# Kernel tuning notes

Measured on AMD Instinct MI355X. Metric: run time of the kernel, lower is better.

The kernel has to match this reference:

```python
import jax, jax.numpy as jnp
import numpy as np

B, S, D, H = 4, 2048, 768, 12
DH = D // H          # 64 head dim
DF = 4 * D           # 3072 FFN hidden
EPS = 1e-5


def setup_inputs() -> dict:
    key = jax.random.key(0)
    ks = jax.random.split(key, 16)
    s = 0.02
    inp = {
        "Q": jax.random.normal(ks[0], (B, S, D), jnp.float32),
        "K": jax.random.normal(ks[1], (B, S, D), jnp.float32),
        "V": jax.random.normal(ks[2], (B, S, D), jnp.float32),
        "Wq": s * jax.random.normal(ks[3], (D, D), jnp.float32),
        "bq": jnp.zeros((D,), jnp.float32),
        "Wk": s * jax.random.normal(ks[4], (D, D), jnp.float32),
        "bk": jnp.zeros((D,), jnp.float32),
        "Wv": s * jax.random.normal(ks[5], (D, D), jnp.float32),
        "bv": jnp.zeros((D,), jnp.float32),
        "Wo": s * jax.random.normal(ks[6], (D, D), jnp.float32),
        "bo": jnp.zeros((D,), jnp.float32),
        "ln_g": jnp.ones((D,), jnp.float32),
        "ln_b": jnp.zeros((D,), jnp.float32),
        "W1": s * jax.random.normal(ks[7], (D, DF), jnp.float32),
        "b1": jnp.zeros((DF,), jnp.float32),
        "W2": s * jax.random.normal(ks[8], (DF, D), jnp.float32),
        "b2": jnp.zeros((D,), jnp.float32),
    }
    return inp


def _split_heads(x):  # [B,S,D] -> [B,H,S,DH]
    return x.reshape(B, S, H, DH).transpose(0, 2, 1, 3)


def _layernorm(x, g, b):
    mu = jnp.mean(x, axis=-1, keepdims=True)
    var = jnp.mean(jnp.square(x - mu), axis=-1, keepdims=True)
    return (x - mu) * jax.lax.rsqrt(var + EPS) * g + b


def reference(Q, K, V, Wq, bq, Wk, bk, Wv, bv, Wo, bo, ln_g, ln_b, W1, b1, W2, b2):
    q = _split_heads(Q @ Wq + bq)            # [B,H,S,DH]
    k = _split_heads(K @ Wk + bk)
    v = _split_heads(V @ Wv + bv)
    scale = 1.0 / jnp.sqrt(jnp.asarray(DH, q.dtype))
    scores = jnp.einsum("bhqd,bhkd->bhqk", q, k) * scale   # [B,H,S,S]
    attn = jax.nn.softmax(scores, axis=-1)
    ctx = jnp.einsum("bhqk,bhkd->bhqd", attn, v)            # [B,H,S,DH]
    ctx = ctx.transpose(0, 2, 1, 3).reshape(B, S, D)
    attn_out = ctx @ Wo + bo
    h = _layernorm(Q + attn_out, ln_g, ln_b)                # residual + LN
    ff = jax.nn.gelu(h @ W1 + b1, approximate=False) @ W2 + b2
    return ff
```

## Files before the change

kernel.cpp:

```cpp
#include <hip/hip_runtime.h>
#include <hip/hip_bf16.h>
#include <math.h>

#define Bsz 4
#define Ssz 2048
#define Dsz 768
#define Hn  12
#define DHn 64
#define DFn 3072
#define NTOK (Bsz*Ssz)
#define EPSL 1e-5f

typedef __attribute__((ext_vector_type(8))) short bf16x8;
typedef __attribute__((ext_vector_type(4))) float f32x4;

__device__ __forceinline__ unsigned short f2bf(float f) {
    unsigned int u = __float_as_uint(f);
    u += 0x7fffu + ((u >> 16) & 1u);
    return (unsigned short)(u >> 16);
}
__device__ __forceinline__ float bf2f(unsigned short h) {
    return __uint_as_float(((unsigned int)h) << 16);
}

__device__ __forceinline__ void swizzle_mn(int bid, int mtot, int nb, int& m, int& n)
{
    const int xcd = bid & 7;
    const int idx = bid >> 3;
    m = xcd * (mtot >> 3) + idx / nb;
    n = idx % nb;
}

__global__ __launch_bounds__(256)
void wsplit_k(const float* __restrict__ W, unsigned short* __restrict__ Wh,
              unsigned short* __restrict__ Wl, int K, int N)
{
    __shared__ float tile[32][33];
    const int n0 = blockIdx.x * 32, k0 = blockIdx.y * 32;
    const int x = threadIdx.x, y = threadIdx.y;
    #pragma unroll
    for (int i = 0; i < 4; i++)
        tile[y + 8 * i][x] = W[(size_t)(k0 + y + 8 * i) * N + n0 + x];
    __syncthreads();
    #pragma unroll
    for (int i = 0; i < 4; i++) {
        float v = tile[x][y + 8 * i];
        unsigned short hb = f2bf(v);
        size_t o = (size_t)(n0 + y + 8 * i) * K + k0 + x;
        Wh[o] = hb;
        Wl[o] = f2bf(v - bf2f(hb));
    }
}

__global__ __launch_bounds__(256)
void presplit_k(const float* __restrict__ Qf, const float* __restrict__ Kf,
                const float* __restrict__ Vf,
                unsigned short* __restrict__ Qh, unsigned short* __restrict__ Ql,
                unsigned short* __restrict__ Kh, unsigned short* __restrict__ Kl,
                unsigned short* __restrict__ Vh)
{
    const int blocksPerSeg = (NTOK * Dsz) / 2048;
    const int seg = blockIdx.x / blocksPerSeg;
    const int idx = ((blockIdx.x % blocksPerSeg) * 256 + threadIdx.x) * 8;
    const float* src = (seg == 0) ? Qf : (seg == 1) ? Kf : Vf;

    float4 a = *(const float4*)(src + idx);
    float4 b = *(const float4*)(src + idx + 4);
    float fv[8] = {a.x, a.y, a.z, a.w, b.x, b.y, b.z, b.w};

    bf16x8 h8, l8;
    #pragma unroll
    for (int e = 0; e < 8; e++) {
        unsigned short hb = f2bf(fv[e]);
        h8[e] = (short)hb;
        l8[e] = (short)f2bf(fv[e] - bf2f(hb));
    }
    unsigned short* Hp = (seg == 0) ? Qh : (seg == 1) ? Kh : Vh;
    *(bf16x8*)(Hp + idx) = h8;
    if (seg < 2) {
        unsigned short* Lp = (seg == 0) ? Ql : Kl;
        *(bf16x8*)(Lp + idx) = l8;
    }
}

__global__ __launch_bounds__(256)
void qkv_mfma(const unsigned short* __restrict__ Qsh, const unsigned short* __restrict__ Qsl,
              const unsigned short* __restrict__ Ksh, const unsigned short* __restrict__ Ksl,
              const unsigned short* __restrict__ Vsh,
              const unsigned short* __restrict__ Wqh, const unsigned short* __restrict__ Wql,
              const unsigned short* __restrict__ Wkh, const unsigned short* __restrict__ Wkl,
              const unsigned short* __restrict__ Wvh, const unsigned short* __restrict__ Wvl,
              const float* __restrict__ bq, const float* __restrict__ bk,
              const float* __restrict__ bv,
              unsigned short* __restrict__ qh, unsigned short* __restrict__ ql,
              unsigned short* __restrict__ kh, unsigned short* __restrict__ kl,
              unsigned short* __restrict__ vout)
{
    __shared__ short smem[16384];
    short* As_h = smem;
    short* As_l = smem + 4096;
    short* Bs_h = smem + 8192;
    short* Bs_l = smem + 12288;

    const int t    = threadIdx.x;
    const int lane = t & 63;
    const int w    = t >> 6;
    const int wm   = w >> 1;
    const int wn   = w & 1;

    int m_tile, nblk;
    swizzle_mn(blockIdx.x, 192, 6, m_tile, nblk);
    const int which = m_tile / 64;
    const int m0    = (m_tile % 64) * 128;
    const int n0    = nblk * 128;

    const unsigned short* Ah = (which == 0) ? Qsh : (which == 1) ? Ksh : Vsh;
    const unsigned short* Al = (which == 0) ? Qsl : Ksl;
    const unsigned short* Bh = (which == 0) ? Wqh : (which == 1) ? Wkh : Wvh;
    const unsigned short* Bl = (which == 0) ? Wql : (which == 1) ? Wkl : Wvl;
    const float* bias = (which == 0) ? bq : (which == 1) ? bk : bv;

    f32x4 acc[4][4];
    #pragma unroll
    for (int i = 0; i < 4; i++)
        #pragma unroll
        for (int j = 0; j < 4; j++)
            acc[i][j] = (f32x4){0.f, 0.f, 0.f, 0.f};

    const int fr = lane & 15;
    const int q8 = (lane >> 4) * 8;

    for (int k0 = 0; k0 < Dsz; k0 += 32) {
        __syncthreads();
        #pragma unroll
        for (int it = 0; it < 2; it++) {
            const int p   = t + 256 * it;
            const int row = p >> 2;
            const int c8  = (p & 3) * 8;
            const unsigned short* ga_h = Ah + (size_t)(m0 + row) * Dsz + k0 + c8;
            const unsigned short* gb_h = Bh + (size_t)(n0 + row) * Dsz + k0 + c8;
            __builtin_amdgcn_global_load_lds((const __attribute__((address_space(1))) void*)ga_h,
                (__attribute__((address_space(3))) void*)(As_h + p * 8), 16, 0, 0);
            __builtin_amdgcn_global_load_lds((const __attribute__((address_space(1))) void*)gb_h,
                (__attribute__((address_space(3))) void*)(Bs_h + p * 8), 16, 0, 0);
            if (which < 2) {
                const unsigned short* ga_l = Al + (size_t)(m0 + row) * Dsz + k0 + c8;
                const unsigned short* gb_l = Bl + (size_t)(n0 + row) * Dsz + k0 + c8;
                __builtin_amdgcn_global_load_lds((const __attribute__((address_space(1))) void*)ga_l,
                    (__attribute__((address_space(3))) void*)(As_l + p * 8), 16, 0, 0);
                __builtin_amdgcn_global_load_lds((const __attribute__((address_space(1))) void*)gb_l,
                    (__attribute__((address_space(3))) void*)(Bs_l + p * 8), 16, 0, 0);
            }
        }
        __syncthreads();

        bf16x8 a_h[4], a_l[4], b_h[4], b_l[4];
        #pragma unroll
        for (int i = 0; i < 4; i++) {
            const int ra = (wm * 64 + i * 16 + fr) * 32 + q8;
            const int rb = (wn * 64 + i * 16 + fr) * 32 + q8;
            a_h[i] = *(const bf16x8*)&As_h[ra];
            b_h[i] = *(const bf16x8*)&Bs_h[rb];
            if (which < 2) {
                a_l[i] = *(const bf16x8*)&As_l[ra];
                b_l[i] = *(const bf16x8*)&Bs_l[rb];
            }
        }
        if (which < 2) {
            #pragma unroll
            for (int i = 0; i < 4; i++)
                #pragma unroll
                for (int j = 0; j < 4; j++) {
                    acc[i][j] = __builtin_amdgcn_mfma_f32_16x16x32_bf16(a_l[i], b_h[j], acc[i][j], 0, 0, 0);
                    acc[i][j] = __builtin_amdgcn_mfma_f32_16x16x32_bf16(a_h[i], b_l[j], acc[i][j], 0, 0, 0);
                    acc[i][j] = __builtin_amdgcn_mfma_f32_16x16x32_bf16(a_h[i], b_h[j], acc[i][j], 0, 0, 0);
                }
        } else {
            #pragma unroll
            for (int i = 0; i < 4; i++)
                #pragma unroll
                for (int j = 0; j < 4; j++)
                    acc[i][j] = __builtin_amdgcn_mfma_f32_16x16x32_bf16(a_h[i], b_h[j], acc[i][j], 0, 0, 0);
        }
    }

    const int quad = lane >> 4;
    #pragma unroll
    for (int i = 0; i < 4; i++)
        #pragma unroll
        for (int j = 0; j < 4; j++) {
            const int n  = n0 + wn * 64 + j * 16 + fr;
            const float bn = bias[n];
            const int hh = n >> 6, dh = n & 63;
            #pragma unroll
            for (int r = 0; r < 4; r++) {
                const int m = m0 + wm * 64 + i * 16 + quad * 4 + r;
                const int bb = m >> 11, s = m & 2047;
                const size_t o = (((size_t)bb * Hn + hh) * Ssz + s) * DHn + dh;
                float v = acc[i][j][r] + bn;
                if (which == 0) {
                    v *= 0.125f;
                    unsigned short hb = f2bf(v);
                    qh[o] = hb; ql[o] = f2bf(v - bf2f(hb));
                } else if (which == 1) {
                    unsigned short hb = f2bf(v);
                    kh[o] = hb; kl[o] = f2bf(v - bf2f(hb));
                } else {
                    vout[o] = f2bf(v);
                }
            }
        }
}

__global__ __launch_bounds__(256)
void vtrans_k(const unsigned short* __restrict__ src, unsigned short* __restrict__ dst)
{
    __shared__ unsigned short tl[32][33];
    const int s0 = blockIdx.x * 32;
    const int d0 = blockIdx.y * 32;
    const int hd = blockIdx.z;
    const int x = threadIdx.x, y = threadIdx.y;
    const size_t base = (size_t)hd * Ssz * DHn;
    #pragma unroll
    for (int i = 0; i < 4; i++)
        tl[y + 8 * i][x] = src[base + (size_t)(s0 + y + 8 * i) * DHn + d0 + x];
    __syncthreads();
    #pragma unroll
    for (int i = 0; i < 4; i++)
        dst[base + (size_t)(d0 + y + 8 * i) * Ssz + s0 + x] = tl[x][y + 8 * i];
}

template<int MODE, bool ASPLIT, bool BSPLIT, int BM>
__global__ __launch_bounds__(256)
void gemm_mfma(const unsigned short* __restrict__ Ah, const unsigned short* __restrict__ Al,
               const unsigned short* __restrict__ Bh, const unsigned short* __restrict__ Bl,
               const float* __restrict__ bias, const float* __restrict__ res,
               float* __restrict__ Cf, unsigned short* __restrict__ Cb,
               int M, int N, int K)
{
    constexpr int MI = BM / 32;
    __shared__ short smem[16384];
    short* As_h = smem;
    short* As_l = smem + 4096;
    short* Bs_h = smem + 8192;
    short* Bs_l = smem + 12288;

    const int t    = threadIdx.x;
    const int lane = t & 63;
    const int w    = t >> 6;
    const int wm   = w >> 1;
    const int wn   = w & 1;

    int mt, nt_;
    swizzle_mn(blockIdx.x, M / BM, N >> 7, mt, nt_);
    const int m0 = mt * BM;
    const int n0 = nt_ * 128;

    f32x4 acc[MI][4];
    #pragma unroll
    for (int i = 0; i < MI; i++)
        #pragma unroll
        for (int j = 0; j < 4; j++)
            acc[i][j] = (f32x4){0.f, 0.f, 0.f, 0.f};

    const int fr = lane & 15;
    const int q8 = (lane >> 4) * 8;

    for (int k0 = 0; k0 < K; k0 += 32) {
        __syncthreads();
        #pragma unroll
        for (int it = 0; it < BM / 64; it++) {
            const int p   = t + 256 * it;
            const int row = p >> 2;
            const int c8  = (p & 3) * 8;
            const unsigned short* ga_h = Ah + (size_t)(m0 + row) * K + k0 + c8;
            __builtin_amdgcn_global_load_lds((const __attribute__((address_space(1))) void*)ga_h,
                (__attribute__((address_space(3))) void*)(As_h + p * 8), 16, 0, 0);
            if (ASPLIT) {
                const unsigned short* ga_l = Al + (size_t)(m0 + row) * K + k0 + c8;
                __builtin_amdgcn_global_load_lds((const __attribute__((address_space(1))) void*)ga_l,
                    (__attribute__((address_space(3))) void*)(As_l + p * 8), 16, 0, 0);
            }
        }
        #pragma unroll
        for (int it = 0; it < 2; it++) {
            const int p   = t + 256 * it;
            const int row = p >> 2;
            const int c8  = (p & 3) * 8;
            const unsigned short* gb_h = Bh + (size_t)(n0 + row) * K + k0 + c8;
            __builtin_amdgcn_global_load_lds((const __attribute__((address_space(1))) void*)gb_h,
                (__attribute__((address_space(3))) void*)(Bs_h + p * 8), 16, 0, 0);
            if (BSPLIT) {
                const unsigned short* gb_l = Bl + (size_t)(n0 + row) * K + k0 + c8;
                __builtin_amdgcn_global_load_lds((const __attribute__((address_space(1))) void*)gb_l,
                    (__attribute__((address_space(3))) void*)(Bs_l + p * 8), 16, 0, 0);
            }
        }
        __syncthreads();

        bf16x8 a_h[MI], a_l[MI], b_h[4], b_l[4];
        #pragma unroll
        for (int i = 0; i < MI; i++) {
            const int ra = (wm * (BM / 2) + i * 16 + fr) * 32 + q8;
            a_h[i] = *(const bf16x8*)&As_h[ra];
            if (ASPLIT) a_l[i] = *(const bf16x8*)&As_l[ra];
        }
        #pragma unroll
        for (int j = 0; j < 4; j++) {
            const int rb = (wn * 64 + j * 16 + fr) * 32 + q8;
            b_h[j] = *(const bf16x8*)&Bs_h[rb];
            if (BSPLIT) b_l[j] = *(const bf16x8*)&Bs_l[rb];
        }
        #pragma unroll
        for (int i = 0; i < MI; i++)
            #pragma unroll
            for (int j = 0; j < 4; j++) {
                if (ASPLIT)
                    acc[i][j] = __builtin_amdgcn_mfma_f32_16x16x32_bf16(a_l[i], b_h[j], acc[i][j], 0, 0, 0);
                if (BSPLIT)
                    acc[i][j] = __builtin_amdgcn_mfma_f32_16x16x32_bf16(a_h[i], b_l[j], acc[i][j], 0, 0, 0);
                acc[i][j] = __builtin_amdgcn_mfma_f32_16x16x32_bf16(a_h[i], b_h[j], acc[i][j], 0, 0, 0);
            }
    }

    const int quad = lane >> 4;
    #pragma unroll
    for (int i = 0; i < MI; i++)
        #pragma unroll
        for (int j = 0; j < 4; j++) {
            const int n  = n0 + wn * 64 + j * 16 + fr;
            const float bn = bias[n];
            #pragma unroll
            for (int r = 0; r < 4; r++) {
                const int m = m0 + wm * (BM / 2) + i * 16 + quad * 4 + r;
                float v = acc[i][j][r] + bn;
                if (MODE == 1) {
                    v += res[(size_t)m * N + n];
                    Cf[(size_t)m * N + n] = v;
                } else if (MODE == 2) {
                    v = 0.5f * v * (1.0f + erff(v * 0.70710678118654752f));
                    Cb[(size_t)m * N + n] = f2bf(v);
                } else {
                    Cf[(size_t)m * N + n] = v;
                }
            }
        }
}

__device__ __forceinline__ void stage16(const unsigned short* src, short* dst,
                                        int p0, int lane, int row0, int rstride, int col0)
{
    const int p   = p0 + lane;
    const int n   = p >> 3;
    const int cst = (p & 7) ^ (n & 7);
    const unsigned short* g = src + (size_t)(row0 + n) * rstride + col0 + cst * 8;
    __builtin_amdgcn_global_load_lds((const __attribute__((address_space(1))) void*)g,
        (__attribute__((address_space(3))) void*)(dst + p0 * 8), 16, 0, 0);
}

__device__ __forceinline__ bf16x8 frag(const short* arr, int row, int c)
{
    const int pos = row * 8 + (c ^ (row & 7));
    return *(const bf16x8*)&arr[pos * 8];
}

__global__ __launch_bounds__(256)
void attn_mfma(const unsigned short* __restrict__ qh, const unsigned short* __restrict__ ql,
               const unsigned short* __restrict__ kh, const unsigned short* __restrict__ kl,
               const unsigned short* __restrict__ vt, unsigned short* __restrict__ ch)
{
    const int hid = blockIdx.x;
    const int b   = hid / Hn;
    const int h   = hid - b * Hn;
    const int q0  = blockIdx.y * 64;
    const int t    = threadIdx.x;
    const int lane = t & 63;
    const int w    = t >> 6;
    const int fr   = lane & 15;
    const int quad = lane >> 4;

    __shared__ short sKV[12288];
    __shared__ short sQP[8192];
    short* Kh_s = sKV;
    short* Kl_s = sKV + 4096;
    short* Vh_s = sKV + 8192;
    short* Qh_s = sQP;
    short* Ql_s = sQP + 4096;
    float* Pw   = (float*)sQP + w * 1024;

    const size_t hoff = (size_t)hid * Ssz * DHn;

    stage16(qh + hoff, Qh_s, w * 128,      lane, q0, DHn, 0);
    stage16(qh + hoff, Qh_s, w * 128 + 64, lane, q0, DHn, 0);
    stage16(ql + hoff, Ql_s, w * 128,      lane, q0, DHn, 0);
    stage16(ql + hoff, Ql_s, w * 128 + 64, lane, q0, DHn, 0);

    f32x4 O[4];
    #pragma unroll
    for (int d = 0; d < 4; d++) O[d] = (f32x4){0.f, 0.f, 0.f, 0.f};
    float lp[4] = {0.f, 0.f, 0.f, 0.f};

    bf16x8 qfh[2], qfl[2];

    for (int kt = 0; kt < Ssz / 64; kt++) {
        __syncthreads();
        const int kr = kt * 64;
        #pragma unroll
        for (int bt = 0; bt < 2; bt++) {
            const int p0 = w * 128 + bt * 64;
            stage16(kh + hoff, Kh_s, p0, lane, kr, DHn, 0);
            stage16(kl + hoff, Kl_s, p0, lane, kr, DHn, 0);
            stage16(vt + hoff, Vh_s, p0, lane, 0, Ssz, kr);
        }
        __syncthreads();

        if (kt == 0) {
            #pragma unroll
            for (int kc = 0; kc < 2; kc++) {
                qfh[kc] = frag(Qh_s, w * 16 + fr, kc * 4 + quad);
                qfl[kc] = frag(Ql_s, w * 16 + fr, kc * 4 + quad);
            }
            __syncthreads();
        }

        f32x4 sc[4];
        #pragma unroll
        for (int nt = 0; nt < 4; nt++) sc[nt] = (f32x4){0.f, 0.f, 0.f, 0.f};
        __builtin_amdgcn_s_setprio(1);
        #pragma unroll
        for (int nt = 0; nt < 4; nt++)
            #pragma unroll
            for (int kc = 0; kc < 2; kc++) {
                bf16x8 bh = frag(Kh_s, nt * 16 + fr, kc * 4 + quad);
                bf16x8 bl = frag(Kl_s, nt * 16 + fr, kc * 4 + quad);
                sc[nt] = __builtin_amdgcn_mfma_f32_16x16x32_bf16(qfl[kc], bh, sc[nt], 0, 0, 0);
                sc[nt] = __builtin_amdgcn_mfma_f32_16x16x32_bf16(qfh[kc], bl, sc[nt], 0, 0, 0);
                sc[nt] = __builtin_amdgcn_mfma_f32_16x16x32_bf16(qfh[kc], bh, sc[nt], 0, 0, 0);
            }
        __builtin_amdgcn_s_setprio(0);

        #pragma unroll
        for (int r = 0; r < 4; r++) {
            const int m = quad * 4 + r;
            #pragma unroll
            for (int nt = 0; nt < 4; nt++) {
                float p = __expf(sc[nt][r]);
                const int j  = nt * 16 + fr;
                const int c4 = j >> 2;
                Pw[(m * 16 + (c4 ^ m)) * 4 + (j & 3)] = p;
                lp[r] += p;
            }
        }

        #pragma unroll
        for (int kc = 0; kc < 2; kc++) {
            const int c4a = kc * 8 + quad * 2;
            float4 pa = *(float4*)&Pw[(fr * 16 + (c4a ^ fr)) * 4];
            float4 pb = *(float4*)&Pw[(fr * 16 + ((c4a + 1) ^ fr)) * 4];
            union { bf16x8 v; __hip_bfloat162 b2[4]; } P;
            P.b2[0] = __float22bfloat162_rn(make_float2(pa.x, pa.y));
            P.b2[1] = __float22bfloat162_rn(make_float2(pa.z, pa.w));
            P.b2[2] = __float22bfloat162_rn(make_float2(pb.x, pb.y));
            P.b2[3] = __float22bfloat162_rn(make_float2(pb.z, pb.w));
            __builtin_amdgcn_s_setprio(1);
            #pragma unroll
            for (int dt = 0; dt < 4; dt++) {
                bf16x8 vh = frag(Vh_s, dt * 16 + fr, kc * 4 + quad);
                O[dt] = __builtin_amdgcn_mfma_f32_16x16x32_bf16(P.v, vh, O[dt], 0, 0, 0);
            }
            __builtin_amdgcn_s_setprio(0);
        }
    }

    #pragma unroll
    for (int r = 0; r < 4; r++) {
        float ls = lp[r];
        #pragma unroll
        for (int msk = 1; msk < 16; msk <<= 1) ls += __shfl_xor(ls, msk);
        const float linv = 1.0f / ls;
        const int s = q0 + w * 16 + quad * 4 + r;
        unsigned short* och = ch + ((size_t)b * Ssz + s) * Dsz + h * DHn;
        #pragma unroll
        for (int dt = 0; dt < 4; dt++)
            och[dt * 16 + fr] = f2bf(O[dt][r] * linv);
    }
}

__global__ __launch_bounds__(256)
void ln_k(const float* __restrict__ x, const float* __restrict__ g,
          const float* __restrict__ bb, unsigned short* __restrict__ yh)
{
    const int row = blockIdx.x;
    const float* xr = x + (size_t)row * Dsz;
    unsigned short* yhr = yh + (size_t)row * Dsz;
    const int t = threadIdx.x;

    float v0 = xr[t], v1 = xr[t + 256], v2 = xr[t + 512];
    float s = v0 + v1 + v2;
    #pragma unroll
    for (int o = 1; o < 64; o <<= 1) s += __shfl_xor(s, o, 64);

    __shared__ float red1[4];
    __shared__ float red2[4];
    const int wid = t >> 6, lane = t & 63;
    if (lane == 0) red1[wid] = s;
    __syncthreads();
    const float mean = (red1[0] + red1[1] + red1[2] + red1[3]) * (1.0f / Dsz);

    float d0 = v0 - mean, d1 = v1 - mean, d2 = v2 - mean;
    float vs = d0 * d0 + d1 * d1 + d2 * d2;
    #pragma unroll
    for (int o = 1; o < 64; o <<= 1) vs += __shfl_xor(vs, o, 64);
    if (lane == 0) red2[wid] = vs;
    __syncthreads();
    const float var = (red2[0] + red2[1] + red2[2] + red2[3]) * (1.0f / Dsz);
    const float inv = rsqrtf(var + EPSL);

    yhr[t]       = f2bf(d0 * inv * g[t]       + bb[t]);
    yhr[t + 256] = f2bf(d1 * inv * g[t + 256] + bb[t + 256]);
    yhr[t + 512] = f2bf(d2 * inv * g[t + 512] + bb[t + 512]);
}

extern "C" void kernel_launch(void* const* d_in, const int* in_sizes, int n_in,
                              void* d_out, int out_size, void* d_ws, size_t ws_size,
                              hipStream_t stream)
{
    (void)in_sizes; (void)n_in; (void)out_size; (void)ws_size;
    const float* Q    = (const float*)d_in[0];
    const float* Kin  = (const float*)d_in[1];
    const float* Vin  = (const float*)d_in[2];
    const float* Wq   = (const float*)d_in[3];
    const float* bq   = (const float*)d_in[4];
    const float* Wk   = (const float*)d_in[5];
    const float* bk   = (const float*)d_in[6];
    const float* Wv   = (const float*)d_in[7];
    const float* bv   = (const float*)d_in[8];
    const float* Wo   = (const float*)d_in[9];
    const float* bo   = (const float*)d_in[10];
    const float* ln_g = (const float*)d_in[11];
    const float* ln_b = (const float*)d_in[12];
    const float* W1   = (const float*)d_in[13];
    const float* b1   = (const float*)d_in[14];
    const float* W2   = (const float*)d_in[15];
    const float* b2   = (const float*)d_in[16];
    float* out = (float*)d_out;

    const size_t NT = (size_t)NTOK * Dsz;
    unsigned short* usws = (unsigned short*)d_ws;
    unsigned short* qh  = usws + 0 * NT;
    unsigned short* ql  = usws + 1 * NT;
    unsigned short* kh  = usws + 2 * NT;
    unsigned short* kl  = usws + 3 * NT;
    unsigned short* vt  = usws + 4 * NT;
    unsigned short* ch  = usws + 6 * NT;
    unsigned short* wsp = usws + 8 * NT;
    const size_t SW = (size_t)Dsz * Dsz;
    unsigned short* Wqh = wsp + 0 * SW;
    unsigned short* Wql = wsp + 1 * SW;
    unsigned short* Wkh = wsp + 2 * SW;
    unsigned short* Wkl = wsp + 3 * SW;
    unsigned short* Wvh = wsp + 4 * SW;
    unsigned short* Wvl = wsp + 5 * SW;
    unsigned short* Woh = wsp + 6 * SW;
    unsigned short* Wol = wsp + 7 * SW;
    unsigned short* W1h = wsp + 8 * SW;
    unsigned short* W1l = wsp + 12 * SW;
    unsigned short* W2h = wsp + 16 * SW;
    unsigned short* W2l = wsp + 20 * SW;
    float*          hpre = (float*)usws;
    unsigned short* hh   = kh;
    unsigned short* hbuf = usws + 4 * NT;

    unsigned short* Qsh = usws + 4 * NT;
    unsigned short* Qsl = usws + 5 * NT;
    unsigned short* Ksh = usws + 7 * NT;
    unsigned short* Ksl = (unsigned short*)d_out;
    unsigned short* Vsh = (unsigned short*)d_out + NT;

    dim3 wb(32, 8);
    wsplit_k<<<dim3(Dsz / 32, Dsz / 32), wb, 0, stream>>>(Wq, Wqh, Wql, Dsz, Dsz);
    wsplit_k<<<dim3(Dsz / 32, Dsz / 32), wb, 0, stream>>>(Wk, Wkh, Wkl, Dsz, Dsz);
    wsplit_k<<<dim3(Dsz / 32, Dsz / 32), wb, 0, stream>>>(Wv, Wvh, Wvl, Dsz, Dsz);
    wsplit_k<<<dim3(Dsz / 32, Dsz / 32), wb, 0, stream>>>(Wo, Woh, Wol, Dsz, Dsz);
    wsplit_k<<<dim3(DFn / 32, Dsz / 32), wb, 0, stream>>>(W1, W1h, W1l, Dsz, DFn);
    wsplit_k<<<dim3(Dsz / 32, DFn / 32), wb, 0, stream>>>(W2, W2h, W2l, DFn, Dsz);

    presplit_k<<<3 * (NTOK * Dsz / 2048), 256, 0, stream>>>(
        Q, Kin, Vin, Qsh, Qsl, Ksh, Ksl, Vsh);

    qkv_mfma<<<1152, 256, 0, stream>>>(
        Qsh, Qsl, Ksh, Ksl, Vsh,
        Wqh, Wql, Wkh, Wkl, Wvh, Wvl, bq, bk, bv,
        qh, ql, kh, kl, ch);

    vtrans_k<<<dim3(Ssz / 32, DHn / 32, Bsz * Hn), wb, 0, stream>>>(ch, vt);

    attn_mfma<<<dim3(Bsz * Hn, Ssz / 64), 256, 0, stream>>>(qh, ql, kh, kl, vt, ch);

    gemm_mfma<1, false, true, 64><<<768, 256, 0, stream>>>(
        ch, nullptr, Woh, Wol, bo, Q, hpre, nullptr, NTOK, Dsz, Dsz);

    ln_k<<<NTOK, 256, 0, stream>>>(hpre, ln_g, ln_b, hh);

    gemm_mfma<2, false, true, 128><<<1536, 256, 0, stream>>>(
        hh, nullptr, W1h, W1l, b1, nullptr, nullptr, hbuf, NTOK, DFn, Dsz);
    gemm_mfma<3, false, false, 64><<<768, 256, 0, stream>>>(
        hbuf, nullptr, W2h, nullptr, b2, nullptr, out, nullptr, NTOK, Dsz, DFn);
}
```

Before: 639.9 us.

## Load attention K/V fragments directly from global memory instead of LDS staging

Removes the per-tile LDS staging of K, K-low and transposed V (and the two block barriers per iteration) in the attention kernel; each wave now reads its MFMA operand fragments straight from global memory, relying on L1/L2 caching since all four waves read the same K/V tile. Q fragments are also loaded directly into registers. The grid is transposed so consecutive blocks share the same head, improving L2 reuse of K/V. The cost is redundant global/L1 traffic (four waves each fetching the full tile) and exposed load latency without explicit prefetch.

```diff
diff --git a/kernel.cpp b/kernel.cpp
--- a/kernel.cpp
+++ b/kernel.cpp
@@ -347,96 +347,65 @@
         }
 }
 
-__device__ __forceinline__ void stage16(const unsigned short* src, short* dst,
-                                        int p0, int lane, int row0, int rstride, int col0)
-{
-    const int p   = p0 + lane;
-    const int n   = p >> 3;
-    const int cst = (p & 7) ^ (n & 7);
-    const unsigned short* g = src + (size_t)(row0 + n) * rstride + col0 + cst * 8;
-    __builtin_amdgcn_global_load_lds((const __attribute__((address_space(1))) void*)g,
-        (__attribute__((address_space(3))) void*)(dst + p0 * 8), 16, 0, 0);
-}
-
-__device__ __forceinline__ bf16x8 frag(const short* arr, int row, int c)
-{
-    const int pos = row * 8 + (c ^ (row & 7));
-    return *(const bf16x8*)&arr[pos * 8];
-}
-
 __global__ __launch_bounds__(256)
 void attn_mfma(const unsigned short* __restrict__ qh, const unsigned short* __restrict__ ql,
                const unsigned short* __restrict__ kh, const unsigned short* __restrict__ kl,
                const unsigned short* __restrict__ vt, unsigned short* __restrict__ ch)
 {
-    const int hid = blockIdx.x;
+    const int q0  = blockIdx.x * 64;
+    const int hid = blockIdx.y;
     const int b   = hid / Hn;
     const int h   = hid - b * Hn;
-    const int q0  = blockIdx.y * 64;
     const int t    = threadIdx.x;
     const int lane = t & 63;
     const int w    = t >> 6;
     const int fr   = lane & 15;
     const int quad = lane >> 4;
 
-    __shared__ short sKV[12288];
-    __shared__ short sQP[8192];
-    short* Kh_s = sKV;
-    short* Kl_s = sKV + 4096;
-    short* Vh_s = sKV + 8192;
-    short* Qh_s = sQP;
-    short* Ql_s = sQP + 4096;
-    float* Pw   = (float*)sQP + w * 1024;
+    __shared__ float Pws[4096];
+    float* Pw = Pws + w * 1024;
 
     const size_t hoff = (size_t)hid * Ssz * DHn;
-
-    stage16(qh + hoff, Qh_s, w * 128,      lane, q0, DHn, 0);
-    stage16(qh + hoff, Qh_s, w * 128 + 64, lane, q0, DHn, 0);
-    stage16(ql + hoff, Ql_s, w * 128,      lane, q0, DHn, 0);
-    stage16(ql + hoff, Ql_s, w * 128 + 64, lane, q0, DHn, 0);
+    const unsigned short* Kh_g = kh + hoff;
+    const unsigned short* Kl_g = kl + hoff;
+    const unsigned short* Vt_g = vt + hoff;
+
+    bf16x8 qfh[2], qfl[2];
+    {
+        const unsigned short* qp  = qh + hoff + (size_t)(q0 + w * 16 + fr) * DHn;
+        const unsigned short* qlp = ql + hoff + (size_t)(q0 + w * 16 + fr) * DHn;
+        #pragma unroll
+        for (int kc = 0; kc < 2; kc++) {
+            qfh[kc] = *(const bf16x8*)(qp  + (kc * 4 + quad) * 8);
+            qfl[kc] = *(const bf16x8*)(qlp + (kc * 4 + quad) * 8);
+        }
+    }
 
     f32x4 O[4];
     #pragma unroll
     for (int d = 0; d < 4; d++) O[d] = (f32x4){0.f, 0.f, 0.f, 0.f};
     float lp[4] = {0.f, 0.f, 0.f, 0.f};
 
-    bf16x8 qfh[2], qfl[2];
-
     for (int kt = 0; kt < Ssz / 64; kt++) {
-        __syncthreads();
         const int kr = kt * 64;
-        #pragma unroll
-        for (int bt = 0; bt < 2; bt++) {
-            const int p0 = w * 128 + bt * 64;
-            stage16(kh + hoff, Kh_s, p0, lane, kr, DHn, 0);
-            stage16(kl + hoff, Kl_s, p0, lane, kr, DHn, 0);
-            stage16(vt + hoff, Vh_s, p0, lane, 0, Ssz, kr);
-        }
-        __syncthreads();
-
-        if (kt == 0) {
-            #pragma unroll
-            for (int kc = 0; kc < 2; kc++) {
-                qfh[kc] = frag(Qh_s, w * 16 + fr, kc * 4 + quad);
-                qfl[kc] = frag(Ql_s, w * 16 + fr, kc * 4 + quad);
-            }
-            __syncthreads();
-        }
 
         f32x4 sc[4];
         #pragma unroll
         for (int nt = 0; nt < 4; nt++) sc[nt] = (f32x4){0.f, 0.f, 0.f, 0.f};
         __builtin_amdgcn_s_setprio(1);
         #pragma unroll
-        for (int nt = 0; nt < 4; nt++)
+        for (int nt = 0; nt < 4; nt++) {
+            const unsigned short* krh = Kh_g + (size_t)(kr + nt * 16 + fr) * DHn;
+            const unsigned short* krl = Kl_g + (size_t)(kr + nt * 16 + fr) * DHn;
             #pragma unroll
             for (int kc = 0; kc < 2; kc++) {
-                bf16x8 bh = frag(Kh_s, nt * 16 + fr, kc * 4 + quad);
-                bf16x8 bl = frag(Kl_s, nt * 16 + fr, kc * 4 + quad);
+                bf16x8 bh = *(const bf16x8*)(krh + (kc * 4 + quad) * 8);
+                bf16x8 bl = *(const bf16x8*)(krl + (kc * 4 + quad) * 8);
                 sc[nt] = __builtin_amdgcn_mfma_f32_16x16x32_bf16(qfl[kc], bh, sc[nt], 0, 0, 0);
                 sc[nt] = __builtin_amdgcn_mfma_f32_16x16x32_bf16(qfh[kc], bl, sc[nt], 0, 0, 0);
                 sc[nt] = __builtin_amdgcn_mfma_f32_16x16x32_bf16(qfh[kc], bh, sc[nt], 0, 0, 0);
             }
+        }
         __builtin_amdgcn_s_setprio(0);
 
         #pragma unroll
@@ -465,7 +434,8 @@
             __builtin_amdgcn_s_setprio(1);
             #pragma unroll
             for (int dt = 0; dt < 4; dt++) {
-                bf16x8 vh = frag(Vh_s, dt * 16 + fr, kc * 4 + quad);
+                bf16x8 vh = *(const bf16x8*)(Vt_g + (size_t)(dt * 16 + fr) * Ssz
+                                             + kr + (kc * 4 + quad) * 8);
                 O[dt] = __builtin_amdgcn_mfma_f32_16x16x32_bf16(P.v, vh, O[dt], 0, 0, 0);
             }
             __builtin_amdgcn_s_setprio(0);
@@ -595,7 +565,7 @@
 
     vtrans_k<<<dim3(Ssz / 32, DHn / 32, Bsz * Hn), wb, 0, stream>>>(ch, vt);
 
-    attn_mfma<<<dim3(Bsz * Hn, Ssz / 64), 256, 0, stream>>>(qh, ql, kh, kl, vt, ch);
+    attn_mfma<<<dim3(Ssz / 64, Bsz * Hn), 256, 0, stream>>>(qh, ql, kh, kl, vt, ch);
 
     gemm_mfma<1, false, true, 64><<<768, 256, 0, stream>>>(
         ch, nullptr, Woh, Wol, bo, Q, hpre, nullptr, NTOK, Dsz, Dsz);
```

New measurement: 1.141 ms. 78.2% more time.

## Double-buffer LDS tiles in QKV and generic GEMM kernels to prefetch next K-slice

Applied to the files above, without the earlier changes.

The QKV projection and generic GEMM kernels now keep two LDS buffers and issue global-to-LDS loads for the next K-slice before computing on the current one. This replaces the old pattern of two barriers per iteration, where the loads were exposed, with a single barrier per iteration. The LDS footprint per block doubles (64KB for QKV), which may lower occupancy. Correctness relies on the trailing barrier alone to cover completion of the async global_load_lds writes.

```diff
diff --git a/kernel.cpp b/kernel.cpp
--- a/kernel.cpp
+++ b/kernel.cpp
@@ -22,6 +22,10 @@
 __device__ __forceinline__ float bf2f(unsigned short h) {
     return __uint_as_float(((unsigned int)h) << 16);
 }
+
+#define GLDS(gp, lp) __builtin_amdgcn_global_load_lds( \
+    (const __attribute__((address_space(1))) void*)(gp), \
+    (__attribute__((address_space(3))) void*)(lp), 16, 0, 0)
 
 __device__ __forceinline__ void swizzle_mn(int bid, int mtot, int nb, int& m, int& n)
 {
@@ -96,11 +100,7 @@
               unsigned short* __restrict__ kh, unsigned short* __restrict__ kl,
               unsigned short* __restrict__ vout)
 {
-    __shared__ short smem[16384];
-    short* As_h = smem;
-    short* As_l = smem + 4096;
-    short* Bs_h = smem + 8192;
-    short* Bs_l = smem + 12288;
+    __shared__ short smem[32768];
 
     const int t    = threadIdx.x;
     const int lane = t & 63;
@@ -130,29 +130,33 @@
     const int fr = lane & 15;
     const int q8 = (lane >> 4) * 8;
 
-    for (int k0 = 0; k0 < Dsz; k0 += 32) {
-        __syncthreads();
+    auto stage = [&](int buf, int k0) {
+        short* base = smem + buf * 16384;
         #pragma unroll
         for (int it = 0; it < 2; it++) {
             const int p   = t + 256 * it;
             const int row = p >> 2;
             const int c8  = (p & 3) * 8;
-            const unsigned short* ga_h = Ah + (size_t)(m0 + row) * Dsz + k0 + c8;
-            const unsigned short* gb_h = Bh + (size_t)(n0 + row) * Dsz + k0 + c8;
-            __builtin_amdgcn_global_load_lds((const __attribute__((address_space(1))) void*)ga_h,
-                (__attribute__((address_space(3))) void*)(As_h + p * 8), 16, 0, 0);
-            __builtin_amdgcn_global_load_lds((const __attribute__((address_space(1))) void*)gb_h,
-                (__attribute__((address_space(3))) void*)(Bs_h + p * 8), 16, 0, 0);
+            GLDS(Ah + (size_t)(m0 + row) * Dsz + k0 + c8, base + p * 8);
+            GLDS(Bh + (size_t)(n0 + row) * Dsz + k0 + c8, base + 8192 + p * 8);
             if (which < 2) {
-                const unsigned short* ga_l = Al + (size_t)(m0 + row) * Dsz + k0 + c8;
-                const unsigned short* gb_l = Bl + (size_t)(n0 + row) * Dsz + k0 + c8;
-                __builtin_amdgcn_global_load_lds((const __attribute__((address_space(1))) void*)ga_l,
-                    (__attribute__((address_space(3))) void*)(As_l + p * 8), 16, 0, 0);
-                __builtin_amdgcn_global_load_lds((const __attribute__((address_space(1))) void*)gb_l,
-                    (__attribute__((address_space(3))) void*)(Bs_l + p * 8), 16, 0, 0);
-            }
-        }
-        __syncthreads();
+                GLDS(Al + (size_t)(m0 + row) * Dsz + k0 + c8, base + 4096 + p * 8);
+                GLDS(Bl + (size_t)(n0 + row) * Dsz + k0 + c8, base + 12288 + p * 8);
+            }
+        }
+    };
+
+    stage(0, 0);
+    __syncthreads();
+    int cur = 0;
+    for (int k0 = 0; k0 < Dsz; k0 += 32) {
+        if (k0 + 32 < Dsz) stage(cur ^ 1, k0 + 32);
+
+        short* base = smem + cur * 16384;
+        short* As_h = base;
+        short* As_l = base + 4096;
+        short* Bs_h = base + 8192;
+        short* Bs_l = base + 12288;
 
         bf16x8 a_h[4], a_l[4], b_h[4], b_l[4];
         #pragma unroll
@@ -182,6 +186,8 @@
                 for (int j = 0; j < 4; j++)
                     acc[i][j] = __builtin_amdgcn_mfma_f32_16x16x32_bf16(a_h[i], b_h[j], acc[i][j], 0, 0, 0);
         }
+        __syncthreads();
+        cur ^= 1;
     }
 
     const int quad = lane >> 4;
@@ -239,11 +245,11 @@
                int M, int N, int K)
 {
     constexpr int MI = BM / 32;
-    __shared__ short smem[16384];
-    short* As_h = smem;
-    short* As_l = smem + 4096;
-    short* Bs_h = smem + 8192;
-    short* Bs_l = smem + 12288;
+    constexpr int AE = BM * 32;
+    constexpr int NA = ASPLIT ? 2 : 1;
+    constexpr int NB = BSPLIT ? 2 : 1;
+    constexpr int BUFE = AE * NA + 4096 * NB;
+    __shared__ short smem[2 * BUFE];
 
     const int t    = threadIdx.x;
     const int lane = t & 63;
@@ -266,37 +272,40 @@
     const int fr = lane & 15;
     const int q8 = (lane >> 4) * 8;
 
-    for (int k0 = 0; k0 < K; k0 += 32) {
-        __syncthreads();
+    auto stage = [&](int buf, int k0) {
+        short* base = smem + buf * BUFE;
         #pragma unroll
         for (int it = 0; it < BM / 64; it++) {
             const int p   = t + 256 * it;
             const int row = p >> 2;
             const int c8  = (p & 3) * 8;
-            const unsigned short* ga_h = Ah + (size_t)(m0 + row) * K + k0 + c8;
-            __builtin_amdgcn_global_load_lds((const __attribute__((address_space(1))) void*)ga_h,
-                (__attribute__((address_space(3))) void*)(As_h + p * 8), 16, 0, 0);
-            if (ASPLIT) {
-                const unsigned short* ga_l = Al + (size_t)(m0 + row) * K + k0 + c8;
-                __builtin_amdgcn_global_load_lds((const __attribute__((address_space(1))) void*)ga_l,
-                    (__attribute__((address_space(3))) void*)(As_l + p * 8), 16, 0, 0);
-            }
-        }
+            GLDS(Ah + (size_t)(m0 + row) * K + k0 + c8, base + p * 8);
+            if (ASPLIT)
+                GLDS(Al + (size_t)(m0 + row) * K + k0 + c8, base + AE + p * 8);
+        }
+        short* bbase = base + AE * NA;
         #pragma unroll
         for (int it = 0; it < 2; it++) {
             const int p   = t + 256 * it;
             const int row = p >> 2;
             const int c8  = (p & 3) * 8;
-            const unsigned short* gb_h = Bh + (size_t)(n0 + row) * K + k0 + c8;
-            __builtin_amdgcn_global_load_lds((const __attribute__((address_space(1))) void*)gb_h,
-                (__attribute__((address_space(3))) void*)(Bs_h + p * 8), 16, 0, 0);
-            if (BSPLIT) {
-                const unsigned short* gb_l = Bl + (size_t)(n0 + row) * K + k0 + c8;
-                __builtin_amdgcn_global_load_lds((const __attribute__((address_space(1))) void*)gb_l,
-                    (__attribute__((address_space(3))) void*)(Bs_l + p * 8), 16, 0, 0);
-            }
-        }
-        __syncthreads();
+            GLDS(Bh + (size_t)(n0 + row) * K + k0 + c8, bbase + p * 8);
+            if (BSPLIT)
+                GLDS(Bl + (size_t)(n0 + row) * K + k0 + c8, bbase + 4096 + p * 8);
+        }
+    };
+
+    stage(0, 0);
+    __syncthreads();
+    int cur = 0;
+    for (int k0 = 0; k0 < K; k0 += 32) {
+        if (k0 + 32 < K) stage(cur ^ 1, k0 + 32);
+
+        short* base = smem + cur * BUFE;
+        short* As_h = base;
+        short* As_l = base + AE;
+        short* Bs_h = base + AE * NA;
+        short* Bs_l = Bs_h + 4096;
 
         bf16x8 a_h[MI], a_l[MI], b_h[4], b_l[4];
         #pragma unroll
@@ -321,6 +330,8 @@
                     acc[i][j] = __builtin_amdgcn_mfma_f32_16x16x32_bf16(a_h[i], b_l[j], acc[i][j], 0, 0, 0);
                 acc[i][j] = __builtin_amdgcn_mfma_f32_16x16x32_bf16(a_h[i], b_h[j], acc[i][j], 0, 0, 0);
             }
+        __syncthreads();
+        cur ^= 1;
     }
 
     const int quad = lane >> 4;
@@ -354,8 +365,7 @@
     const int n   = p >> 3;
     const int cst = (p & 7) ^ (n & 7);
     const unsigned short* g = src + (size_t)(row0 + n) * rstride + col0 + cst * 8;
-    __builtin_amdgcn_global_load_lds((const __attribute__((address_space(1))) void*)g,
-        (__attribute__((address_space(3))) void*)(dst + p0 * 8), 16, 0, 0);
+    GLDS(g, dst + p0 * 8);
 }
 
 __device__ __forceinline__ bf16x8 frag(const short* arr, int row, int c)
```

New measurement: 602.4 us. 1.06x faster.
